# Kernel tuning notes

Hardware: AMD Instinct MI355X
Metric: run time of the kernel (lower is better)

## Reference

```python
import jax, jax.numpy as jnp
import numpy as np

N = 100000   # nodes
E = 1600000  # edges (avg degree 16)
IN = 128     # in_size == out_size (required by layer stacking)
H = 4        # heads
D = 32       # per-head dim = out_size / heads
L = 3        # n_layers
NEG_SLOPE = 0.2  # DGL GATConv default leaky_relu slope


def setup_inputs() -> dict:
    key = jax.random.key(0)
    ks = jax.random.split(key, 7)
    h = jax.random.normal(ks[0], (N, IN), dtype=jnp.float32)
    src = jax.random.randint(ks[1], (E,), 0, N, dtype=jnp.int32)
    dst = jax.random.randint(ks[2], (E,), 0, N, dtype=jnp.int32)
    Ws = jax.random.normal(ks[3], (L, IN, H * D), dtype=jnp.float32) * 0.05
    attn_l = jax.random.normal(ks[4], (L, H, D), dtype=jnp.float32) * 0.05
    attn_r = jax.random.normal(ks[5], (L, H, D), dtype=jnp.float32) * 0.05
    bias = jnp.zeros((L, H, D), dtype=jnp.float32)
    return {"h": h, "src": src, "dst": dst, "Ws": Ws,
            "attn_l": attn_l, "attn_r": attn_r, "bias": bias}


def _gat_layer(h, src, dst, W, al, ar, b):
    # linear projection (no bias), reshape to heads
    ft = (h @ W).reshape(N, H, D)                       # [N,H,D]
    el = jnp.einsum('nhd,hd->nh', ft, al)               # [N,H]
    er = jnp.einsum('nhd,hd->nh', ft, ar)               # [N,H]
    # edge attention logits
    e = jax.nn.leaky_relu(el[src] + er[dst], NEG_SLOPE)  # [E,H]
    # segment softmax over incoming edges of each destination node
    m = jax.ops.segment_max(e, dst, num_segments=N)     # [N,H]
    m = jnp.where(jnp.isfinite(m), m, jnp.zeros_like(m))  # zero in-degree guard
    ee = jnp.exp(e - m[dst])                            # [E,H]
    den = jax.ops.segment_sum(ee, dst, num_segments=N)  # [N,H]
    a = ee / jnp.maximum(den[dst], 1e-9)                # [E,H]
    # weighted scatter-sum of source messages
    rst = jax.ops.segment_sum(ft[src] * a[:, :, None], dst, num_segments=N)  # [N,H,D]
    # residual (Identity: in_feats == H*D), bias, ELU activation
    rst = rst + h.reshape(N, H, D) + b
    return jax.nn.elu(rst), a


def reference(h, src, dst, Ws, attn_l, attn_r, bias):
    x = h
    a = None
    for i in range(L):
        out, a = _gat_layer(x, src, dst, Ws[i], attn_l[i], attn_r[i], bias[i])
        x = out.reshape(N, H * D)  # flatten(1)
    return x, a[:, :, None]  # ([N, H*D], [E, H, 1]) as DGL returns
```

## Files before the change

kernel.cpp:

```cpp
#include <hip/hip_runtime.h>
#include <hip/hip_bf16.h>
#include <math.h>

#define NN 100000
#define EE 1600000
#define IN_F 128
#define HH 4
#define DD 32
#define LL 3
#define NB_ 391
#define EPB 4096

typedef __bf16 bf16x8 __attribute__((ext_vector_type(8)));
typedef float f32x4 __attribute__((ext_vector_type(4)));

static __device__ __forceinline__ unsigned short f2bf(float x) {
    __hip_bfloat16 b = __float2bfloat16(x);
    return *reinterpret_cast<unsigned short*>(&b);
}

__global__ void convert_h_kernel(const float* __restrict__ x,
                                 unsigned short* __restrict__ xb) {
    const int i = blockIdx.x * blockDim.x + threadIdx.x;
    if (i >= NN * 32) return;
    const float4 v = ((const float4*)x)[i];
    ushort4 o;
    o.x = f2bf(v.x); o.y = f2bf(v.y); o.z = f2bf(v.z); o.w = f2bf(v.w);
    ((ushort4*)xb)[i] = o;
}

__global__ void wt_kernel(const float* __restrict__ Ws,
                          unsigned short* __restrict__ wt) {
    const int i = blockIdx.x * blockDim.x + threadIdx.x;
    if (i >= LL * IN_F * IN_F) return;
    const int l = i >> 14, r = i & 16383;
    const int n = r >> 7, k = r & 127;
    wt[i] = f2bf(Ws[(l << 14) + k * IN_F + n]);
}

__global__ __launch_bounds__(256) void gemm_mfma_kernel(
    const unsigned short* __restrict__ x_bf,
    const unsigned short* __restrict__ wt,
    const float* __restrict__ al,
    const float* __restrict__ ar,
    unsigned short* __restrict__ ft_bf,
    float* __restrict__ el,
    float* __restrict__ er) {
    const int wave = (blockIdx.x * blockDim.x + threadIdx.x) >> 6;
    const int lane = threadIdx.x & 63;
    const int base = wave * 16;
    if (base >= NN) return;
    const int c = lane & 15;
    const int quad = lane >> 4;

    const int arow = min(base + c, NN - 1);
    const bf16x8* ap = (const bf16x8*)(x_bf + (size_t)arow * IN_F);
    bf16x8 a[4];
#pragma unroll
    for (int kc = 0; kc < 4; ++kc) a[kc] = ap[kc * 4 + quad];

    f32x4 acc[8];
#pragma unroll
    for (int nt = 0; nt < 8; ++nt) {
        const bf16x8* bp = (const bf16x8*)(wt + (size_t)(nt * 16 + c) * IN_F);
        f32x4 d = {0.f, 0.f, 0.f, 0.f};
#pragma unroll
        for (int kc = 0; kc < 4; ++kc)
            d = __builtin_amdgcn_mfma_f32_16x16x32_bf16(a[kc], bp[kc * 4 + quad], d, 0, 0, 0);
        acc[nt] = d;
    }

#pragma unroll
    for (int r = 0; r < 4; ++r) {
        const int n = base + quad * 4 + r;
        if (n < NN) {
#pragma unroll
            for (int nt = 0; nt < 8; ++nt)
                ft_bf[(size_t)n * IN_F + nt * 16 + c] = f2bf(acc[nt][r]);
        }
    }

#pragma unroll
    for (int h = 0; h < 4; ++h) {
        float pl[4], pr[4];
#pragma unroll
        for (int r = 0; r < 4; ++r) {
            const float a0 = acc[2 * h][r], a1 = acc[2 * h + 1][r];
            pl[r] = a0 * al[h * 32 + c] + a1 * al[h * 32 + 16 + c];
            pr[r] = a0 * ar[h * 32 + c] + a1 * ar[h * 32 + 16 + c];
        }
#pragma unroll
        for (int off = 8; off >= 1; off >>= 1) {
#pragma unroll
            for (int r = 0; r < 4; ++r) {
                pl[r] += __shfl_xor(pl[r], off);
                pr[r] += __shfl_xor(pr[r], off);
            }
        }
        if (c == 0) {
#pragma unroll
            for (int r = 0; r < 4; ++r) {
                const int n = base + quad * 4 + r;
                if (n < NN) {
                    el[n * HH + h] = pl[r];
                    er[n * HH + h] = pr[r];
                }
            }
        }
    }
}


__global__ void bucket_hist_kernel(const int* __restrict__ dst,
                                   int* __restrict__ tot) {
    __shared__ int l[NB_];
    for (int b = threadIdx.x; b < NB_; b += 256) l[b] = 0;
    __syncthreads();
    const int e0 = blockIdx.x * EPB;
    const int e1 = min(e0 + EPB, EE);
    for (int e = e0 + threadIdx.x; e < e1; e += 256)
        atomicAdd(&l[dst[e] >> 8], 1);
    __syncthreads();
    for (int b = threadIdx.x; b < NB_; b += 256)
        if (l[b]) atomicAdd(&tot[b], l[b]);
}

__global__ void bucket_scan_kernel(const int* __restrict__ tot,
                                   int* __restrict__ base,
                                   int* __restrict__ cur) {
    __shared__ int tmp[512];
    const int tid = threadIdx.x;
    int v = (tid < NB_) ? tot[tid] : 0;
    tmp[tid] = v;
    __syncthreads();
    for (int off = 1; off < 512; off <<= 1) {
        int t = (tid >= off) ? tmp[tid - off] : 0;
        __syncthreads();
        if (tid >= off) tmp[tid] += t;
        __syncthreads();
    }
    if (tid < NB_) {
        const int excl = tmp[tid] - v;
        base[tid] = excl;
        cur[tid] = excl;
    }
    if (tid == 0) base[NB_] = EE;
}

__global__ void partition_kernel(const int* __restrict__ src,
                                 const int* __restrict__ dst,
                                 int* __restrict__ cur,
                                 int* __restrict__ bkt) {
    __shared__ int lcnt[NB_];
    __shared__ int lbase[NB_];
    const int tid = threadIdx.x;
    const int e0 = blockIdx.x * EPB;
    const int e1 = min(e0 + EPB, EE);
    for (int b = tid; b < NB_; b += 256) lcnt[b] = 0;
    __syncthreads();
    for (int e = e0 + tid; e < e1; e += 256)
        atomicAdd(&lcnt[dst[e] >> 8], 1);
    __syncthreads();
    for (int b = tid; b < NB_; b += 256) {
        const int c = lcnt[b];
        lbase[b] = c ? atomicAdd(&cur[b], c) : 0;
        lcnt[b] = 0;
    }
    __syncthreads();
    for (int e = e0 + tid; e < e1; e += 256) {
        const int d = dst[e];
        const int b = d >> 8;
        const int idx = atomicAdd(&lcnt[b], 1);
        bkt[lbase[b] + idx] = ((d & 255) << 17) | src[e];
    }
}

__global__ void bucket_sort_kernel(const int* __restrict__ bkt,
                                   const int* __restrict__ base,
                                   int* __restrict__ cnt,
                                   int* __restrict__ row_start,
                                   int* __restrict__ ssrc) {
    __shared__ int lcnt[256];
    __shared__ int loff[256];
    const int tid = threadIdx.x;
    const int b = blockIdx.x;
    const int s0 = base[b], s1 = base[b + 1];
    lcnt[tid] = 0;
    __syncthreads();
    for (int p = s0 + tid; p < s1; p += 256)
        atomicAdd(&lcnt[bkt[p] >> 17], 1);
    __syncthreads();
    const int v = lcnt[tid];
    loff[tid] = v;
    __syncthreads();
    for (int off = 1; off < 256; off <<= 1) {
        int t = (tid >= off) ? loff[tid - off] : 0;
        __syncthreads();
        if (tid >= off) loff[tid] += t;
        __syncthreads();
    }
    const int excl = loff[tid] - v;
    const int n = b * 256 + tid;
    if (n < NN) {
        cnt[n] = v;
        row_start[n] = s0 + excl;
    }
    __syncthreads();
    loff[tid] = excl;
    lcnt[tid] = 0;
    __syncthreads();
    for (int p = s0 + tid; p < s1; p += 256) {
        const int w = bkt[p];
        const int dl = w >> 17;
        const int idx = atomicAdd(&lcnt[dl], 1);
        ssrc[s0 + loff[dl] + idx] = w & 0x1FFFF;
    }
}

__global__ void aggregate_kernel(const unsigned int* __restrict__ ftw,
                                 const float* __restrict__ el,
                                 const float* __restrict__ er,
                                 const float* __restrict__ xin,
                                 const float* __restrict__ bias,
                                 const int* __restrict__ row_start,
                                 const int* __restrict__ cnt,
                                 const int* __restrict__ ssrc,
                                 float* __restrict__ out,
                                 unsigned short* __restrict__ out_bf,
                                 float* __restrict__ den_arr) {
    const int n = (blockIdx.x * blockDim.x + threadIdx.x) >> 6;
    const int lane = threadIdx.x & 63;
    if (n >= NN) return;
    const int h = lane >> 4;

    const float ern = er[n * HH + h];
    float acc0 = 0.f, acc1 = 0.f, den = 0.f;
    const int beg = row_start[n];
    const int end = beg + cnt[n];

    int p = beg;
    for (; p + 4 <= end; p += 4) {
        int s[4];
#pragma unroll
        for (int j = 0; j < 4; ++j) s[j] = ssrc[p + j];
        float ee[4];
        unsigned int w[4];
#pragma unroll
        for (int j = 0; j < 4; ++j) {
            float ev = el[s[j] * HH + h] + ern;
            ev = ev > 0.f ? ev : 0.2f * ev;
            ee[j] = __expf(ev);
            w[j] = ftw[(size_t)s[j] * 64 + lane];
        }
#pragma unroll
        for (int j = 0; j < 4; ++j) {
            den += ee[j];
            acc0 = fmaf(ee[j], __uint_as_float(w[j] << 16), acc0);
            acc1 = fmaf(ee[j], __uint_as_float(w[j] & 0xffff0000u), acc1);
        }
    }
    for (; p < end; ++p) {
        const int s = ssrc[p];
        float ev = el[s * HH + h] + ern;
        ev = ev > 0.f ? ev : 0.2f * ev;
        const float e1 = __expf(ev);
        den += e1;
        const unsigned int w = ftw[(size_t)s * 64 + lane];
        acc0 = fmaf(e1, __uint_as_float(w << 16), acc0);
        acc1 = fmaf(e1, __uint_as_float(w & 0xffff0000u), acc1);
    }

    if ((lane & 15) == 0) den_arr[n * HH + h] = den;

    const float inv = 1.f / fmaxf(den, 1e-9f);
    const float2 xi = ((const float2*)xin)[(size_t)n * 64 + lane];
    float v0 = acc0 * inv + xi.x + bias[2 * lane];
    float v1 = acc1 * inv + xi.y + bias[2 * lane + 1];
    v0 = v0 > 0.f ? v0 : __expf(v0) - 1.f;
    v1 = v1 > 0.f ? v1 : __expf(v1) - 1.f;
    ((float2*)out)[(size_t)n * 64 + lane] = make_float2(v0, v1);
    ushort2 ob;
    ob.x = f2bf(v0); ob.y = f2bf(v1);
    ((ushort2*)out_bf)[(size_t)n * 64 + lane] = ob;
}

__global__ void attn_out_kernel(const int* __restrict__ src,
                                const int* __restrict__ dst,
                                const float* __restrict__ el,
                                const float* __restrict__ er,
                                const float* __restrict__ den,
                                float* __restrict__ a_out) {
    const int e = blockIdx.x * blockDim.x + threadIdx.x;
    if (e >= EE) return;
    const int s = src[e], d = dst[e];
    const float4 l4 = ((const float4*)el)[s];
    const float4 r4 = ((const float4*)er)[d];
    const float4 dn = ((const float4*)den)[d];
    float v[4] = {l4.x + r4.x, l4.y + r4.y, l4.z + r4.z, l4.w + r4.w};
    float dv[4] = {dn.x, dn.y, dn.z, dn.w};
    float4 o;
    float* op = &o.x;
#pragma unroll
    for (int hh = 0; hh < 4; ++hh) {
        float t = v[hh] > 0.f ? v[hh] : 0.2f * v[hh];
        op[hh] = __expf(t) / fmaxf(dv[hh], 1e-9f);
    }
    ((float4*)a_out)[e] = o;
}

extern "C" void kernel_launch(void* const* d_in, const int* in_sizes, int n_in,
                              void* d_out, int out_size, void* d_ws, size_t ws_size,
                              hipStream_t stream) {
    const float* h    = (const float*)d_in[0];
    const int*   src  = (const int*)  d_in[1];
    const int*   dst  = (const int*)  d_in[2];
    const float* Ws   = (const float*)d_in[3];
    const float* al   = (const float*)d_in[4];
    const float* ar   = (const float*)d_in[5];
    const float* bias = (const float*)d_in[6];

    float* out_x = (float*)d_out;
    float* out_a = out_x + (size_t)NN * IN_F;
    unsigned short* x_bf = (unsigned short*)out_a;

    char* ws = (char*)d_ws;
    unsigned short* ft_bf = (unsigned short*)ws;
    float* bufA = (float*)(ft_bf + (size_t)NN * IN_F);
    float* el   = bufA + (size_t)NN * IN_F;
    float* er   = el + (size_t)NN * HH;
    float* den  = er + (size_t)NN * HH;
    int*   cnt        = (int*)(den + (size_t)NN * HH);
    int*   row_start  = cnt + NN;
    int*   bucket_tot = row_start + NN;
    int*   bucket_base= bucket_tot + 512;
    int*   bucket_cur = bucket_base + 512;
    int*   ssrc       = bucket_cur + 512;
    unsigned short* wt = (unsigned short*)(ssrc + EE);
    int* bkt = (int*)bufA;

    convert_h_kernel<<<(NN * 32 + 255) / 256, 256, 0, stream>>>(h, x_bf);
    wt_kernel<<<(LL * IN_F * IN_F + 255) / 256, 256, 0, stream>>>(Ws, wt);

    hipMemsetAsync(bucket_tot, 0, 512 * sizeof(int), stream);
    const int ebks = (EE + EPB - 1) / EPB;
    bucket_hist_kernel<<<ebks, 256, 0, stream>>>(dst, bucket_tot);
    bucket_scan_kernel<<<1, 512, 0, stream>>>(bucket_tot, bucket_base, bucket_cur);
    partition_kernel<<<ebks, 256, 0, stream>>>(src, dst, bucket_cur, bkt);
    bucket_sort_kernel<<<NB_, 256, 0, stream>>>(bkt, bucket_base, cnt, row_start, ssrc);

    const float* xin[LL]  = {h, bufA, out_x};
    float*       xout[LL] = {bufA, out_x, out_x};
    const int gemm_blocks = ((NN + 15) / 16 + 3) / 4;

    for (int i = 0; i < LL; ++i) {
        const float* all_ = al + (size_t)i * HH * DD;
        const float* arl = ar + (size_t)i * HH * DD;
        const float* bl  = bias + (size_t)i * HH * DD;

        gemm_mfma_kernel<<<gemm_blocks, 256, 0, stream>>>(
            x_bf, wt + (size_t)i * IN_F * IN_F, all_, arl, ft_bf, el, er);
        aggregate_kernel<<<(NN + 3) / 4, 256, 0, stream>>>(
            (const unsigned int*)ft_bf, el, er, xin[i], bl, row_start, cnt, ssrc,
            xout[i], x_bf, den);
    }
    attn_out_kernel<<<(EE + 255) / 256, 256, 0, stream>>>(src, dst, el, er, den, out_a);
}
```

Before: 619.6 us.

## Slice aggregation by feature columns, transpose el, fuse input bf16 conversion into GEMM

```diff
diff --git a/kernel.cpp b/kernel.cpp
--- a/kernel.cpp
+++ b/kernel.cpp
@@ -13,20 +13,11 @@
 
 typedef __bf16 bf16x8 __attribute__((ext_vector_type(8)));
 typedef float f32x4 __attribute__((ext_vector_type(4)));
+typedef unsigned int u32x2 __attribute__((ext_vector_type(2)));
 
 static __device__ __forceinline__ unsigned short f2bf(float x) {
     __hip_bfloat16 b = __float2bfloat16(x);
     return *reinterpret_cast<unsigned short*>(&b);
-}
-
-__global__ void convert_h_kernel(const float* __restrict__ x,
-                                 unsigned short* __restrict__ xb) {
-    const int i = blockIdx.x * blockDim.x + threadIdx.x;
-    if (i >= NN * 32) return;
-    const float4 v = ((const float4*)x)[i];
-    ushort4 o;
-    o.x = f2bf(v.x); o.y = f2bf(v.y); o.z = f2bf(v.z); o.w = f2bf(v.w);
-    ((ushort4*)xb)[i] = o;
 }
 
 __global__ void wt_kernel(const float* __restrict__ Ws,
@@ -38,13 +29,14 @@
     wt[i] = f2bf(Ws[(l << 14) + k * IN_F + n]);
 }
 
+template <bool F32A>
 __global__ __launch_bounds__(256) void gemm_mfma_kernel(
-    const unsigned short* __restrict__ x_bf,
+    const void* __restrict__ a_src,
     const unsigned short* __restrict__ wt,
     const float* __restrict__ al,
     const float* __restrict__ ar,
     unsigned short* __restrict__ ft_bf,
-    float* __restrict__ el,
+    float* __restrict__ elT,
     float* __restrict__ er) {
     const int wave = (blockIdx.x * blockDim.x + threadIdx.x) >> 6;
     const int lane = threadIdx.x & 63;
@@ -54,10 +46,25 @@
     const int quad = lane >> 4;
 
     const int arow = min(base + c, NN - 1);
-    const bf16x8* ap = (const bf16x8*)(x_bf + (size_t)arow * IN_F);
     bf16x8 a[4];
-#pragma unroll
-    for (int kc = 0; kc < 4; ++kc) a[kc] = ap[kc * 4 + quad];
+    if (F32A) {
+        const float4* xp = (const float4*)((const float*)a_src + (size_t)arow * IN_F);
+#pragma unroll
+        for (int kc = 0; kc < 4; ++kc) {
+            const float4 lo = xp[(kc * 4 + quad) * 2];
+            const float4 hi = xp[(kc * 4 + quad) * 2 + 1];
+            union { unsigned short us[8]; bf16x8 v; } u;
+            u.us[0] = f2bf(lo.x); u.us[1] = f2bf(lo.y);
+            u.us[2] = f2bf(lo.z); u.us[3] = f2bf(lo.w);
+            u.us[4] = f2bf(hi.x); u.us[5] = f2bf(hi.y);
+            u.us[6] = f2bf(hi.z); u.us[7] = f2bf(hi.w);
+            a[kc] = u.v;
+        }
+    } else {
+        const bf16x8* ap = (const bf16x8*)((const unsigned short*)a_src + (size_t)arow * IN_F);
+#pragma unroll
+        for (int kc = 0; kc < 4; ++kc) a[kc] = ap[kc * 4 + quad];
+    }
 
     f32x4 acc[8];
 #pragma unroll
@@ -102,7 +109,7 @@
             for (int r = 0; r < 4; ++r) {
                 const int n = base + quad * 4 + r;
                 if (n < NN) {
-                    el[n * HH + h] = pl[r];
+                    elT[(size_t)h * NN + n] = pl[r];
                     er[n * HH + h] = pr[r];
                 }
             }
@@ -217,86 +224,97 @@
     }
 }
 
-__global__ void aggregate_kernel(const unsigned int* __restrict__ ftw,
-                                 const float* __restrict__ el,
-                                 const float* __restrict__ er,
-                                 const float* __restrict__ xin,
-                                 const float* __restrict__ bias,
-                                 const int* __restrict__ row_start,
-                                 const int* __restrict__ cnt,
-                                 const int* __restrict__ ssrc,
-                                 float* __restrict__ out,
-                                 unsigned short* __restrict__ out_bf,
-                                 float* __restrict__ den_arr) {
-    const int n = (blockIdx.x * blockDim.x + threadIdx.x) >> 6;
+__global__ __launch_bounds__(256) void aggregate_slice_kernel(
+    const u32x2* __restrict__ ft2,
+    const float* __restrict__ elT,
+    const float* __restrict__ er,
+    const float* __restrict__ xin,
+    const float* __restrict__ bias,
+    const int* __restrict__ row_start,
+    const int* __restrict__ cnt,
+    const int* __restrict__ ssrc,
+    float* __restrict__ out,
+    unsigned short* __restrict__ out_bf,
+    float* __restrict__ den_arr) {
+    const int slice = blockIdx.x & 7;
+    const int nb = blockIdx.x >> 3;
+    const int n = nb * 4 + (threadIdx.x >> 6);
+    if (n >= NN) return;
     const int lane = threadIdx.x & 63;
-    if (n >= NN) return;
-    const int h = lane >> 4;
+    const int g = lane >> 2;
+    const int fl = lane & 3;
+    const int col = slice * 4 + fl;
+    const int h = slice >> 1;
 
     const float ern = er[n * HH + h];
-    float acc0 = 0.f, acc1 = 0.f, den = 0.f;
     const int beg = row_start[n];
     const int end = beg + cnt[n];
-
-    int p = beg;
-    for (; p + 4 <= end; p += 4) {
-        int s[4];
-#pragma unroll
-        for (int j = 0; j < 4; ++j) s[j] = ssrc[p + j];
-        float ee[4];
-        unsigned int w[4];
-#pragma unroll
-        for (int j = 0; j < 4; ++j) {
-            float ev = el[s[j] * HH + h] + ern;
-            ev = ev > 0.f ? ev : 0.2f * ev;
-            ee[j] = __expf(ev);
-            w[j] = ftw[(size_t)s[j] * 64 + lane];
-        }
-#pragma unroll
-        for (int j = 0; j < 4; ++j) {
-            den += ee[j];
-            acc0 = fmaf(ee[j], __uint_as_float(w[j] << 16), acc0);
-            acc1 = fmaf(ee[j], __uint_as_float(w[j] & 0xffff0000u), acc1);
-        }
-    }
-    for (; p < end; ++p) {
-        const int s = ssrc[p];
-        float ev = el[s * HH + h] + ern;
+    const float* elh = elT + (size_t)h * NN;
+
+    float acc0 = 0.f, acc1 = 0.f, acc2 = 0.f, acc3 = 0.f, den = 0.f;
+
+    for (int p0 = beg; p0 < end; p0 += 16) {
+        const int p = p0 + g;
+        const bool valid = p < end;
+        const int s = __builtin_nontemporal_load(&ssrc[valid ? p : beg]);
+        float ev = elh[s] + ern;
+        const u32x2 w = ft2[(size_t)s * 32 + col];
         ev = ev > 0.f ? ev : 0.2f * ev;
-        const float e1 = __expf(ev);
+        const float e1 = valid ? __expf(ev) : 0.f;
         den += e1;
-        const unsigned int w = ftw[(size_t)s * 64 + lane];
-        acc0 = fmaf(e1, __uint_as_float(w << 16), acc0);
-        acc1 = fmaf(e1, __uint_as_float(w & 0xffff0000u), acc1);
-    }
-
-    if ((lane & 15) == 0) den_arr[n * HH + h] = den;
-
-    const float inv = 1.f / fmaxf(den, 1e-9f);
-    const float2 xi = ((const float2*)xin)[(size_t)n * 64 + lane];
-    float v0 = acc0 * inv + xi.x + bias[2 * lane];
-    float v1 = acc1 * inv + xi.y + bias[2 * lane + 1];
-    v0 = v0 > 0.f ? v0 : __expf(v0) - 1.f;
-    v1 = v1 > 0.f ? v1 : __expf(v1) - 1.f;
-    ((float2*)out)[(size_t)n * 64 + lane] = make_float2(v0, v1);
-    ushort2 ob;
-    ob.x = f2bf(v0); ob.y = f2bf(v1);
-    ((ushort2*)out_bf)[(size_t)n * 64 + lane] = ob;
+        acc0 = fmaf(e1, __uint_as_float(w.x << 16), acc0);
+        acc1 = fmaf(e1, __uint_as_float(w.x & 0xffff0000u), acc1);
+        acc2 = fmaf(e1, __uint_as_float(w.y << 16), acc2);
+        acc3 = fmaf(e1, __uint_as_float(w.y & 0xffff0000u), acc3);
+    }
+
+#pragma unroll
+    for (int off = 4; off < 64; off <<= 1) {
+        den  += __shfl_xor(den, off);
+        acc0 += __shfl_xor(acc0, off);
+        acc1 += __shfl_xor(acc1, off);
+        acc2 += __shfl_xor(acc2, off);
+        acc3 += __shfl_xor(acc3, off);
+    }
+
+    if (g == 0) {
+        if (fl == 0 && (slice & 1) == 0) den_arr[n * HH + h] = den;
+        const float inv = 1.f / fmaxf(den, 1e-9f);
+        const f32x4 xi = __builtin_nontemporal_load(
+            (const f32x4*)xin + (size_t)n * 32 + col);
+        const f32x4 bb = ((const f32x4*)bias)[col];
+        float v0 = acc0 * inv + xi.x + bb.x;
+        float v1 = acc1 * inv + xi.y + bb.y;
+        float v2 = acc2 * inv + xi.z + bb.z;
+        float v3 = acc3 * inv + xi.w + bb.w;
+        v0 = v0 > 0.f ? v0 : __expf(v0) - 1.f;
+        v1 = v1 > 0.f ? v1 : __expf(v1) - 1.f;
+        v2 = v2 > 0.f ? v2 : __expf(v2) - 1.f;
+        v3 = v3 > 0.f ? v3 : __expf(v3) - 1.f;
+        f32x4 o = {v0, v1, v2, v3};
+        __builtin_nontemporal_store(o, (f32x4*)out + (size_t)n * 32 + col);
+        const unsigned int lo = (unsigned int)f2bf(v0) | ((unsigned int)f2bf(v1) << 16);
+        const unsigned int hi = (unsigned int)f2bf(v2) | ((unsigned int)f2bf(v3) << 16);
+        u32x2 ob = {lo, hi};
+        __builtin_nontemporal_store(ob, (u32x2*)out_bf + (size_t)n * 32 + col);
+    }
 }
 
 __global__ void attn_out_kernel(const int* __restrict__ src,
                                 const int* __restrict__ dst,
-                                const float* __restrict__ el,
+                                const float* __restrict__ elT,
                                 const float* __restrict__ er,
                                 const float* __restrict__ den,
                                 float* __restrict__ a_out) {
     const int e = blockIdx.x * blockDim.x + threadIdx.x;
     if (e >= EE) return;
     const int s = src[e], d = dst[e];
-    const float4 l4 = ((const float4*)el)[s];
     const float4 r4 = ((const float4*)er)[d];
     const float4 dn = ((const float4*)den)[d];
-    float v[4] = {l4.x + r4.x, l4.y + r4.y, l4.z + r4.z, l4.w + r4.w};
+    float v[4] = {elT[s] + r4.x,
+                  elT[NN + s] + r4.y,
+                  elT[2 * NN + s] + r4.z,
+                  elT[3 * NN + s] + r4.w};
     float dv[4] = {dn.x, dn.y, dn.z, dn.w};
     float4 o;
     float* op = &o.x;
@@ -326,8 +344,8 @@
     char* ws = (char*)d_ws;
     unsigned short* ft_bf = (unsigned short*)ws;
     float* bufA = (float*)(ft_bf + (size_t)NN * IN_F);
-    float* el   = bufA + (size_t)NN * IN_F;
-    float* er   = el + (size_t)NN * HH;
+    float* elT  = bufA + (size_t)NN * IN_F;
+    float* er   = elT + (size_t)NN * HH;
     float* den  = er + (size_t)NN * HH;
     int*   cnt        = (int*)(den + (size_t)NN * HH);
     int*   row_start  = cnt + NN;
@@ -338,7 +356,6 @@
     unsigned short* wt = (unsigned short*)(ssrc + EE);
     int* bkt = (int*)bufA;
 
-    convert_h_kernel<<<(NN * 32 + 255) / 256, 256, 0, stream>>>(h, x_bf);
     wt_kernel<<<(LL * IN_F * IN_F + 255) / 256, 256, 0, stream>>>(Ws, wt);
 
     hipMemsetAsync(bucket_tot, 0, 512 * sizeof(int), stream);
@@ -351,17 +368,23 @@
     const float* xin[LL]  = {h, bufA, out_x};
     float*       xout[LL] = {bufA, out_x, out_x};
     const int gemm_blocks = ((NN + 15) / 16 + 3) / 4;
+    const int agg_blocks  = 8 * ((NN + 3) / 4);
 
     for (int i = 0; i < LL; ++i) {
         const float* all_ = al + (size_t)i * HH * DD;
         const float* arl = ar + (size_t)i * HH * DD;
         const float* bl  = bias + (size_t)i * HH * DD;
 
-        gemm_mfma_kernel<<<gemm_blocks, 256, 0, stream>>>(
-            x_bf, wt + (size_t)i * IN_F * IN_F, all_, arl, ft_bf, el, er);
-        aggregate_kernel<<<(NN + 3) / 4, 256, 0, stream>>>(
-            (const unsigned int*)ft_bf, el, er, xin[i], bl, row_start, cnt, ssrc,
+        if (i == 0) {
+            gemm_mfma_kernel<true><<<gemm_blocks, 256, 0, stream>>>(
+                (const void*)h, wt + (size_t)i * IN_F * IN_F, all_, arl, ft_bf, elT, er);
+        } else {
+            gemm_mfma_kernel<false><<<gemm_blocks, 256, 0, stream>>>(
+                (const void*)x_bf, wt + (size_t)i * IN_F * IN_F, all_, arl, ft_bf, elT, er);
+        }
+        aggregate_slice_kernel<<<agg_blocks, 256, 0, stream>>>(
+            (const u32x2*)ft_bf, elT, er, xin[i], bl, row_start, cnt, ssrc,
             xout[i], x_bf, den);
     }
-    attn_out_kernel<<<(EE + 255) / 256, 256, 0, stream>>>(src, dst, el, er, den, out_a);
-}
+    attn_out_kernel<<<(EE + 255) / 256, 256, 0, stream>>>(src, dst, elT, er, den, out_a);
+}
```

After: 1.571 ms. 153% more time.

## Gather four edges per wave with 16-byte loads and fuse input bf16 conversion

Applied to the files above, without the earlier changes.

```diff
diff --git a/kernel.cpp b/kernel.cpp
--- a/kernel.cpp
+++ b/kernel.cpp
@@ -19,16 +19,6 @@
     return *reinterpret_cast<unsigned short*>(&b);
 }
 
-__global__ void convert_h_kernel(const float* __restrict__ x,
-                                 unsigned short* __restrict__ xb) {
-    const int i = blockIdx.x * blockDim.x + threadIdx.x;
-    if (i >= NN * 32) return;
-    const float4 v = ((const float4*)x)[i];
-    ushort4 o;
-    o.x = f2bf(v.x); o.y = f2bf(v.y); o.z = f2bf(v.z); o.w = f2bf(v.w);
-    ((ushort4*)xb)[i] = o;
-}
-
 __global__ void wt_kernel(const float* __restrict__ Ws,
                           unsigned short* __restrict__ wt) {
     const int i = blockIdx.x * blockDim.x + threadIdx.x;
@@ -38,8 +28,9 @@
     wt[i] = f2bf(Ws[(l << 14) + k * IN_F + n]);
 }
 
+template <bool F32A>
 __global__ __launch_bounds__(256) void gemm_mfma_kernel(
-    const unsigned short* __restrict__ x_bf,
+    const void* __restrict__ a_src,
     const unsigned short* __restrict__ wt,
     const float* __restrict__ al,
     const float* __restrict__ ar,
@@ -54,10 +45,25 @@
     const int quad = lane >> 4;
 
     const int arow = min(base + c, NN - 1);
-    const bf16x8* ap = (const bf16x8*)(x_bf + (size_t)arow * IN_F);
     bf16x8 a[4];
-#pragma unroll
-    for (int kc = 0; kc < 4; ++kc) a[kc] = ap[kc * 4 + quad];
+    if (F32A) {
+        const float4* xp = (const float4*)((const float*)a_src + (size_t)arow * IN_F);
+#pragma unroll
+        for (int kc = 0; kc < 4; ++kc) {
+            const float4 lo = xp[(kc * 4 + quad) * 2];
+            const float4 hi = xp[(kc * 4 + quad) * 2 + 1];
+            union { unsigned short us[8]; bf16x8 v; } u;
+            u.us[0] = f2bf(lo.x); u.us[1] = f2bf(lo.y);
+            u.us[2] = f2bf(lo.z); u.us[3] = f2bf(lo.w);
+            u.us[4] = f2bf(hi.x); u.us[5] = f2bf(hi.y);
+            u.us[6] = f2bf(hi.z); u.us[7] = f2bf(hi.w);
+            a[kc] = u.v;
+        }
+    } else {
+        const bf16x8* ap = (const bf16x8*)((const unsigned short*)a_src + (size_t)arow * IN_F);
+#pragma unroll
+        for (int kc = 0; kc < 4; ++kc) a[kc] = ap[kc * 4 + quad];
+    }
 
     f32x4 acc[8];
 #pragma unroll
@@ -217,7 +223,7 @@
     }
 }
 
-__global__ void aggregate_kernel(const unsigned int* __restrict__ ftw,
+__global__ void aggregate_kernel(const uint4* __restrict__ ft4,
                                  const float* __restrict__ el,
                                  const float* __restrict__ er,
                                  const float* __restrict__ xin,
@@ -231,57 +237,103 @@
     const int n = (blockIdx.x * blockDim.x + threadIdx.x) >> 6;
     const int lane = threadIdx.x & 63;
     if (n >= NN) return;
-    const int h = lane >> 4;
+    const int e4 = lane >> 4;
+    const int fq = lane & 15;
+    const int h = fq >> 2;
 
     const float ern = er[n * HH + h];
-    float acc0 = 0.f, acc1 = 0.f, den = 0.f;
     const int beg = row_start[n];
     const int end = beg + cnt[n];
 
+    float acc[8] = {0.f, 0.f, 0.f, 0.f, 0.f, 0.f, 0.f, 0.f};
+    float den = 0.f;
+
+#define ACC8(E, W)                                                        \
+    acc[0] = fmaf(E, __uint_as_float((W).x << 16), acc[0]);               \
+    acc[1] = fmaf(E, __uint_as_float((W).x & 0xffff0000u), acc[1]);       \
+    acc[2] = fmaf(E, __uint_as_float((W).y << 16), acc[2]);               \
+    acc[3] = fmaf(E, __uint_as_float((W).y & 0xffff0000u), acc[3]);       \
+    acc[4] = fmaf(E, __uint_as_float((W).z << 16), acc[4]);               \
+    acc[5] = fmaf(E, __uint_as_float((W).z & 0xffff0000u), acc[5]);       \
+    acc[6] = fmaf(E, __uint_as_float((W).w << 16), acc[6]);               \
+    acc[7] = fmaf(E, __uint_as_float((W).w & 0xffff0000u), acc[7]);
+
     int p = beg;
-    for (; p + 4 <= end; p += 4) {
-        int s[4];
-#pragma unroll
-        for (int j = 0; j < 4; ++j) s[j] = ssrc[p + j];
-        float ee[4];
-        unsigned int w[4];
-#pragma unroll
-        for (int j = 0; j < 4; ++j) {
-            float ev = el[s[j] * HH + h] + ern;
-            ev = ev > 0.f ? ev : 0.2f * ev;
-            ee[j] = __expf(ev);
-            w[j] = ftw[(size_t)s[j] * 64 + lane];
-        }
-#pragma unroll
-        for (int j = 0; j < 4; ++j) {
-            den += ee[j];
-            acc0 = fmaf(ee[j], __uint_as_float(w[j] << 16), acc0);
-            acc1 = fmaf(ee[j], __uint_as_float(w[j] & 0xffff0000u), acc1);
-        }
-    }
-    for (; p < end; ++p) {
-        const int s = ssrc[p];
+    for (; p + 16 <= end; p += 16) {
+        const int s0 = ssrc[p + e4];
+        const int s1 = ssrc[p + 4 + e4];
+        const int s2 = ssrc[p + 8 + e4];
+        const int s3 = ssrc[p + 12 + e4];
+        float ev0 = el[s0 * HH + h] + ern;
+        float ev1 = el[s1 * HH + h] + ern;
+        float ev2 = el[s2 * HH + h] + ern;
+        float ev3 = el[s3 * HH + h] + ern;
+        const uint4 w0 = ft4[(size_t)s0 * 16 + fq];
+        const uint4 w1 = ft4[(size_t)s1 * 16 + fq];
+        const uint4 w2 = ft4[(size_t)s2 * 16 + fq];
+        const uint4 w3 = ft4[(size_t)s3 * 16 + fq];
+        ev0 = ev0 > 0.f ? ev0 : 0.2f * ev0;
+        ev1 = ev1 > 0.f ? ev1 : 0.2f * ev1;
+        ev2 = ev2 > 0.f ? ev2 : 0.2f * ev2;
+        ev3 = ev3 > 0.f ? ev3 : 0.2f * ev3;
+        const float e0 = __expf(ev0);
+        const float e1 = __expf(ev1);
+        const float e2 = __expf(ev2);
+        const float e3 = __expf(ev3);
+        den += (e0 + e1) + (e2 + e3);
+        ACC8(e0, w0)
+        ACC8(e1, w1)
+        ACC8(e2, w2)
+        ACC8(e3, w3)
+    }
+    for (; p < end; p += 4) {
+        const int pe = p + e4;
+        const bool valid = pe < end;
+        const int s = ssrc[valid ? pe : beg];
         float ev = el[s * HH + h] + ern;
+        const uint4 w = ft4[(size_t)s * 16 + fq];
         ev = ev > 0.f ? ev : 0.2f * ev;
-        const float e1 = __expf(ev);
+        const float e1 = valid ? __expf(ev) : 0.f;
         den += e1;
-        const unsigned int w = ftw[(size_t)s * 64 + lane];
-        acc0 = fmaf(e1, __uint_as_float(w << 16), acc0);
-        acc1 = fmaf(e1, __uint_as_float(w & 0xffff0000u), acc1);
-    }
-
-    if ((lane & 15) == 0) den_arr[n * HH + h] = den;
-
-    const float inv = 1.f / fmaxf(den, 1e-9f);
-    const float2 xi = ((const float2*)xin)[(size_t)n * 64 + lane];
-    float v0 = acc0 * inv + xi.x + bias[2 * lane];
-    float v1 = acc1 * inv + xi.y + bias[2 * lane + 1];
-    v0 = v0 > 0.f ? v0 : __expf(v0) - 1.f;
-    v1 = v1 > 0.f ? v1 : __expf(v1) - 1.f;
-    ((float2*)out)[(size_t)n * 64 + lane] = make_float2(v0, v1);
-    ushort2 ob;
-    ob.x = f2bf(v0); ob.y = f2bf(v1);
-    ((ushort2*)out_bf)[(size_t)n * 64 + lane] = ob;
+        ACC8(e1, w)
+    }
+#undef ACC8
+
+#pragma unroll
+    for (int off = 16; off < 64; off <<= 1) {
+        den += __shfl_xor(den, off);
+#pragma unroll
+        for (int k = 0; k < 8; ++k) acc[k] += __shfl_xor(acc[k], off);
+    }
+
+    if (lane < 16) {
+        if ((fq & 3) == 0) den_arr[n * HH + h] = den;
+        const float inv = 1.f / fmaxf(den, 1e-9f);
+        const float4 xi0 = ((const float4*)xin)[(size_t)n * 32 + fq * 2];
+        const float4 xi1 = ((const float4*)xin)[(size_t)n * 32 + fq * 2 + 1];
+        const float4 bb0 = ((const float4*)bias)[fq * 2];
+        const float4 bb1 = ((const float4*)bias)[fq * 2 + 1];
+        float v[8];
+        v[0] = acc[0] * inv + xi0.x + bb0.x;
+        v[1] = acc[1] * inv + xi0.y + bb0.y;
+        v[2] = acc[2] * inv + xi0.z + bb0.z;
+        v[3] = acc[3] * inv + xi0.w + bb0.w;
+        v[4] = acc[4] * inv + xi1.x + bb1.x;
+        v[5] = acc[5] * inv + xi1.y + bb1.y;
+        v[6] = acc[6] * inv + xi1.z + bb1.z;
+        v[7] = acc[7] * inv + xi1.w + bb1.w;
+#pragma unroll
+        for (int k = 0; k < 8; ++k)
+            v[k] = v[k] > 0.f ? v[k] : __expf(v[k]) - 1.f;
+        ((float4*)out)[(size_t)n * 32 + fq * 2] = make_float4(v[0], v[1], v[2], v[3]);
+        ((float4*)out)[(size_t)n * 32 + fq * 2 + 1] = make_float4(v[4], v[5], v[6], v[7]);
+        uint4 ob;
+        ob.x = (unsigned int)f2bf(v[0]) | ((unsigned int)f2bf(v[1]) << 16);
+        ob.y = (unsigned int)f2bf(v[2]) | ((unsigned int)f2bf(v[3]) << 16);
+        ob.z = (unsigned int)f2bf(v[4]) | ((unsigned int)f2bf(v[5]) << 16);
+        ob.w = (unsigned int)f2bf(v[6]) | ((unsigned int)f2bf(v[7]) << 16);
+        ((uint4*)out_bf)[(size_t)n * 16 + fq] = ob;
+    }
 }
 
 __global__ void attn_out_kernel(const int* __restrict__ src,
@@ -338,7 +390,6 @@
     unsigned short* wt = (unsigned short*)(ssrc + EE);
     int* bkt = (int*)bufA;
 
-    convert_h_kernel<<<(NN * 32 + 255) / 256, 256, 0, stream>>>(h, x_bf);
     wt_kernel<<<(LL * IN_F * IN_F + 255) / 256, 256, 0, stream>>>(Ws, wt);
 
     hipMemsetAsync(bucket_tot, 0, 512 * sizeof(int), stream);
@@ -357,10 +408,15 @@
         const float* arl = ar + (size_t)i * HH * DD;
         const float* bl  = bias + (size_t)i * HH * DD;
 
-        gemm_mfma_kernel<<<gemm_blocks, 256, 0, stream>>>(
-            x_bf, wt + (size_t)i * IN_F * IN_F, all_, arl, ft_bf, el, er);
+        if (i == 0) {
+            gemm_mfma_kernel<true><<<gemm_blocks, 256, 0, stream>>>(
+                (const void*)h, wt + (size_t)i * IN_F * IN_F, all_, arl, ft_bf, el, er);
+        } else {
+            gemm_mfma_kernel<false><<<gemm_blocks, 256, 0, stream>>>(
+                (const void*)x_bf, wt + (size_t)i * IN_F * IN_F, all_, arl, ft_bf, el, er);
+        }
         aggregate_kernel<<<(NN + 3) / 4, 256, 0, stream>>>(
-            (const unsigned int*)ft_bf, el, er, xin[i], bl, row_start, cnt, ssrc,
+            (const uint4*)ft_bf, el, er, xin[i], bl, row_start, cnt, ssrc,
             xout[i], x_bf, den);
     }
     attn_out_kernel<<<(EE + 255) / 256, 256, 0, stream>>>(src, dst, el, er, den, out_a);
```

New measurement: 583.2 us. -5.9%, faster.
